# Kernel optimization log

Hardware: AMD Instinct MI355X
Metric: run time of the kernel (lower is better)

## Reference

```python
import jax, jax.numpy as jnp
import numpy as np

D_MODEL = 1024
BULK_DIM = 10          # int(log2(d_model))
ADS_RADIUS = 1.0
B, N = 4, 2048


def setup_inputs() -> dict:
    key = jax.random.key(0)
    k1, k2 = jax.random.split(key, 2)
    boundary_tokens = jax.random.normal(k1, (B, N, D_MODEL), dtype=jnp.float32)
    W_b2b = jax.random.normal(k2, (D_MODEL, D_MODEL * BULK_DIM), dtype=jnp.float32) / np.sqrt(D_MODEL).astype(np.float32)
    b_b2b = jnp.zeros((D_MODEL * BULK_DIM,), dtype=jnp.float32)
    return {"boundary_tokens": boundary_tokens, "W_b2b": W_b2b, "b_b2b": b_b2b}


def _fast_marching(bulk_coords, ads_radius):
    # bulk_coords: (B, N, K, D). Sequential eikonal-style sweep through the
    # bulk depth z = 1..K; AdS warp factor L/z attenuates the front update
    # deeper into the bulk. Returns geodesics with the same shape.
    cz = jnp.moveaxis(bulk_coords, 2, 0)                 # (K, B, N, D)
    z = jnp.arange(1, bulk_coords.shape[2] + 1, dtype=bulk_coords.dtype)
    factors = ads_radius / z                             # (K,)

    def step(g, inp):
        c, f = inp
        g_new = g + f * (c - g)
        return g_new, g_new

    _, geos = jax.lax.scan(step, cz[0], (cz, factors))   # (K, B, N, D)
    return jnp.moveaxis(geos, 0, 2)                      # (B, N, K, D)


def reference(boundary_tokens, W_b2b, b_b2b):
    Bb, Nn, D = boundary_tokens.shape
    # boundary -> bulk linear projection, reshaped to (B, N, bulk_dim, D)
    bulk_coords = (boundary_tokens @ W_b2b + b_b2b).reshape(Bb, Nn, BULK_DIM, D)
    geodesics = _fast_marching(bulk_coords, ADS_RADIUS)  # (B, N, K, D)
    bulk_features = geodesics.mean(axis=2)               # (B, N, D)
    return bulk_features
```

## Files before the change

kernel.cpp:

```cpp
#include <hip/hip_runtime.h>
#include <stdint.h>


static constexpr float FW[10] = {
    0.2928968253968254f, 0.1928968253968254f, 0.1428968253968254f,
    0.1095634920634921f, 0.0845634920634921f, 0.0645634920634921f,
    0.0478968253968254f, 0.0336111111111111f, 0.0211111111111111f,
    0.0100000000000000f};

typedef __attribute__((ext_vector_type(8))) short short8;
typedef __attribute__((ext_vector_type(4))) float floatx4;

__device__ inline unsigned int bf16pack2(float hi, float lo) {
    unsigned int uh = __float_as_uint(hi) + 0x8000u;
    unsigned int ul = __float_as_uint(lo) + 0x8000u;
    return __builtin_amdgcn_perm(uh, ul, 0x07060302u);
}

#define LDS_AS(p) ((__attribute__((address_space(3))) unsigned int*)(p))
#define GLB_AS(p) ((const __attribute__((address_space(1))) unsigned int*)(p))

__global__ __launch_bounds__(256) void fold_w(const float* __restrict__ W,
                                              unsigned short* __restrict__ Wt) {
    __shared__ float T[32 * 65];
    const int t = threadIdx.x;
    const int n0 = blockIdx.x * 64;
    const int k0 = blockIdx.y * 32;

#pragma unroll
    for (int s = 0; s < 2; ++s) {
        int slot = s * 256 + t;
        int r = slot >> 4;
        int c4 = (slot & 15) * 4;
        const float4* src = (const float4*)(W + (size_t)(k0 + r) * 10240 + n0 + c4);
        float4 acc = {0.f, 0.f, 0.f, 0.f};
#pragma unroll
        for (int j = 0; j < 10; ++j) {
            float4 v = src[j * 256];
            acc.x += FW[j] * v.x; acc.y += FW[j] * v.y;
            acc.z += FW[j] * v.z; acc.w += FW[j] * v.w;
        }
        T[r * 65 + c4 + 0] = acc.x;
        T[r * 65 + c4 + 1] = acc.y;
        T[r * 65 + c4 + 2] = acc.z;
        T[r * 65 + c4 + 3] = acc.w;
    }
    __syncthreads();
#pragma unroll
    for (int s = 0; s < 2; ++s) {
        int slot = s * 256 + t;
        int nl = slot >> 3;
        int k4 = (slot & 7) * 4;
        float f0 = T[(k4 + 0) * 65 + nl];
        float f1 = T[(k4 + 1) * 65 + nl];
        float f2 = T[(k4 + 2) * 65 + nl];
        float f3 = T[(k4 + 3) * 65 + nl];
        uint2 p;
        p.x = bf16pack2(f1, f0);
        p.y = bf16pack2(f3, f2);
        *(uint2*)(Wt + (size_t)(n0 + nl) * 1024 + k0 + k4) = p;
    }
}

__global__ __launch_bounds__(256) void fold_b(const float* __restrict__ b,
                                              float* __restrict__ beff) {
    const int t = threadIdx.x;
    const float4* src = (const float4*)b + t;
    float4 acc = {0.f, 0.f, 0.f, 0.f};
#pragma unroll
    for (int j = 0; j < 10; ++j) {
        float4 v = src[j * 256];
        acc.x += FW[j] * v.x; acc.y += FW[j] * v.y;
        acc.z += FW[j] * v.z; acc.w += FW[j] * v.w;
    }
    ((float4*)beff)[t] = acc;
}

__global__ __launch_bounds__(256) void cvt_bf16(const float* __restrict__ A,
                                                uint4* __restrict__ Ab) {
    size_t i = (size_t)blockIdx.x * 256 + threadIdx.x;
    const float4* src = (const float4*)A + i * 2;
    float4 a0 = src[0], a1 = src[1];
    uint4 p;
    p.x = bf16pack2(a0.y, a0.x);
    p.y = bf16pack2(a0.w, a0.z);
    p.z = bf16pack2(a1.y, a1.x);
    p.w = bf16pack2(a1.w, a1.z);
    Ab[i] = p;
}

__global__ __launch_bounds__(256) void gemm_bf16(const unsigned short* __restrict__ Ab,
                                                 const unsigned short* __restrict__ Wt,
                                                 const float* __restrict__ beff,
                                                 float* __restrict__ C) {
    __shared__ __align__(16) unsigned char As[16384];
    __shared__ __align__(16) unsigned char Bs[16384];

    const int t = threadIdx.x;
    const int lane = t & 63;
    const int w = t >> 6;
    const int quad = lane >> 4;
    const int l15 = lane & 15;
    const int wm = (w & 1) * 64;
    const int wn = (w >> 1) * 64;
    const int bm = blockIdx.x * 128;
    const int bn = blockIdx.y * 128;

    floatx4 acc[4][4];
#pragma unroll
    for (int i = 0; i < 4; ++i)
#pragma unroll
        for (int j = 0; j < 4; ++j) acc[i][j] = (floatx4){0.f, 0.f, 0.f, 0.f};

    const char* Abase = (const char*)Ab + (size_t)bm * 2048;
    const char* Bbase = (const char*)Wt + (size_t)bn * 2048;

    for (int k0 = 0; k0 < 1024; k0 += 64) {
#pragma unroll
        for (int i = 0; i < 4; ++i) {
            int I = w * 4 + i;
            int slot = I * 64 + lane;
            int m = slot >> 3;
            int c = (slot & 7) ^ (m & 7);
            size_t off = (size_t)m * 2048 + (size_t)k0 * 2 + c * 16;
            __builtin_amdgcn_global_load_lds(GLB_AS(Abase + off), LDS_AS(As + I * 1024), 16, 0, 0);
            __builtin_amdgcn_global_load_lds(GLB_AS(Bbase + off), LDS_AS(Bs + I * 1024), 16, 0, 0);
        }
        __syncthreads();

#pragma unroll
        for (int kk = 0; kk < 2; ++kk) {
            short8 af[4], bf[4];
            int c = kk * 4 + quad;
#pragma unroll
            for (int tm = 0; tm < 4; ++tm) {
                int m = wm + tm * 16 + l15;
                int slot = m * 8 + (c ^ (m & 7));
                af[tm] = *(const short8*)(As + slot * 16);
            }
#pragma unroll
            for (int tn = 0; tn < 4; ++tn) {
                int n = wn + tn * 16 + l15;
                int slot = n * 8 + (c ^ (n & 7));
                bf[tn] = *(const short8*)(Bs + slot * 16);
            }
#pragma unroll
            for (int tm = 0; tm < 4; ++tm)
#pragma unroll
                for (int tn = 0; tn < 4; ++tn)
                    acc[tm][tn] = __builtin_amdgcn_mfma_f32_16x16x32_bf16(
                        af[tm], bf[tn], acc[tm][tn], 0, 0, 0);
        }
        __syncthreads();
    }

#pragma unroll
    for (int tn = 0; tn < 4; ++tn) {
        int col = bn + wn + tn * 16 + l15;
        float bias = beff[col];
#pragma unroll
        for (int tm = 0; tm < 4; ++tm) {
            int row0 = bm + wm + tm * 16 + quad * 4;
#pragma unroll
            for (int r = 0; r < 4; ++r)
                C[(size_t)(row0 + r) * 1024 + col] = acc[tm][tn][r] + bias;
        }
    }
}

__global__ __launch_bounds__(256) void gemm_fb(const float* __restrict__ A,
                                               const unsigned short* __restrict__ Wt,
                                               const float* __restrict__ beff,
                                               float* __restrict__ C) {
    __shared__ __align__(16) unsigned short As[128 * 72];
    __shared__ __align__(16) unsigned char Bs[16384];

    const int t = threadIdx.x;
    const int lane = t & 63;
    const int w = t >> 6;
    const int quad = lane >> 4;
    const int l15 = lane & 15;
    const int wm = (w & 1) * 64;
    const int wn = (w >> 1) * 64;
    const int bm = blockIdx.y * 128;
    const int bn = blockIdx.x * 128;

    floatx4 acc[4][4];
#pragma unroll
    for (int i = 0; i < 4; ++i)
#pragma unroll
        for (int j = 0; j < 4; ++j) acc[i][j] = (floatx4){0.f, 0.f, 0.f, 0.f};

    const int ar = t >> 4;
    const int ac4 = (t & 15) * 4;
    const float* Abase = A + (size_t)(bm + ar) * 1024 + ac4;
    const char* WtB = (const char*)Wt;

    for (int k0 = 0; k0 < 1024; k0 += 64) {
#pragma unroll
        for (int i = 0; i < 4; ++i) {
            int I = w * 4 + i;
            int slot = I * 64 + lane;
            int nl = slot >> 3;
            int c = (slot & 7) ^ (nl & 7);
            const char* g = WtB + (size_t)(bn + nl) * 2048 + k0 * 2 + c * 16;
            __builtin_amdgcn_global_load_lds(GLB_AS(g), LDS_AS(Bs + I * 1024), 16, 0, 0);
        }
        float4 av[8];
#pragma unroll
        for (int s = 0; s < 8; ++s)
            av[s] = *(const float4*)(Abase + (size_t)(s * 16) * 1024 + k0);
#pragma unroll
        for (int s = 0; s < 8; ++s) {
            uint2 p;
            p.x = bf16pack2(av[s].y, av[s].x);
            p.y = bf16pack2(av[s].w, av[s].z);
            *(uint2*)((char*)As + (size_t)(s * 16 + ar) * 144 + ac4 * 2) = p;
        }
        __syncthreads();
#pragma unroll
        for (int kk = 0; kk < 2; ++kk) {
            short8 af[4], bf[4];
#pragma unroll
            for (int tm = 0; tm < 4; ++tm) {
                int m = wm + tm * 16 + l15;
                af[tm] = *(const short8*)((const char*)As + (size_t)m * 144 + kk * 64 + quad * 16);
            }
#pragma unroll
            for (int tn = 0; tn < 4; ++tn) {
                int n = wn + tn * 16 + l15;
                int c = kk * 4 + quad;
                int slot = n * 8 + (c ^ (n & 7));
                bf[tn] = *(const short8*)(Bs + slot * 16);
            }
#pragma unroll
            for (int tm = 0; tm < 4; ++tm)
#pragma unroll
                for (int tn = 0; tn < 4; ++tn)
                    acc[tm][tn] = __builtin_amdgcn_mfma_f32_16x16x32_bf16(
                        af[tm], bf[tn], acc[tm][tn], 0, 0, 0);
        }
        __syncthreads();
    }
#pragma unroll
    for (int tn = 0; tn < 4; ++tn) {
        int col = bn + wn + tn * 16 + l15;
        float bias = beff[col];
#pragma unroll
        for (int tm = 0; tm < 4; ++tm) {
            int row0 = bm + wm + tm * 16 + quad * 4;
#pragma unroll
            for (int r = 0; r < 4; ++r)
                C[(size_t)(row0 + r) * 1024 + col] = acc[tm][tn][r] + bias;
        }
    }
}

extern "C" void kernel_launch(void* const* d_in, const int* in_sizes, int n_in,
                              void* d_out, int out_size, void* d_ws, size_t ws_size,
                              hipStream_t stream) {
    const float* tokens = (const float*)d_in[0];
    const float* W      = (const float*)d_in[1];
    const float* b      = (const float*)d_in[2];
    float* out = (float*)d_out;

    unsigned short* Wt = (unsigned short*)d_ws;
    float* beff = (float*)((char*)d_ws + 2097152);
    unsigned short* Ab = (unsigned short*)((char*)d_ws + 2101248);

    fold_w<<<dim3(16, 32), 256, 0, stream>>>(W, Wt);
    fold_b<<<1, 256, 0, stream>>>(b, beff);

    if (ws_size >= 2101248 + (size_t)8192 * 1024 * 2) {
        cvt_bf16<<<4096, 256, 0, stream>>>(tokens, (uint4*)Ab);
        gemm_bf16<<<dim3(64, 8), 256, 0, stream>>>(Ab, Wt, beff, out);
    } else {
        gemm_fb<<<dim3(8, 64), 256, 0, stream>>>(tokens, Wt, beff, out);
    }
}
```

Before: 135.8 us.

## Merge prep kernels into one launch and switch GEMM to 32x32x16 MFMA

Folds the three preprocessing kernels (weight fold/transpose, bias fold, token bf16 conversion) into a single launch that dispatches on block index, removing two kernel launches. The GEMM moves from 16x16x32 to 32x32x16 bf16 MFMA tiles with 2x2 accumulators per wave, which halves the LDS fragment reads per MFMA and cuts the instruction count. In exchange, the epilogue stores are more scattered across rows, and the larger accumulators use more registers.

```diff
diff --git a/kernel.cpp b/kernel.cpp
--- a/kernel.cpp
+++ b/kernel.cpp
@@ -10,6 +10,7 @@
 
 typedef __attribute__((ext_vector_type(8))) short short8;
 typedef __attribute__((ext_vector_type(4))) float floatx4;
+typedef __attribute__((ext_vector_type(16))) float floatx16;
 
 __device__ inline unsigned int bf16pack2(float hi, float lo) {
     unsigned int uh = __float_as_uint(hi) + 0x8000u;
@@ -20,19 +21,57 @@
 #define LDS_AS(p) ((__attribute__((address_space(3))) unsigned int*)(p))
 #define GLB_AS(p) ((const __attribute__((address_space(1))) unsigned int*)(p))
 
-__global__ __launch_bounds__(256) void fold_w(const float* __restrict__ W,
-                                              unsigned short* __restrict__ Wt) {
+__global__ __launch_bounds__(256) void prep(const float* __restrict__ W,
+                                            const float* __restrict__ tokens,
+                                            const float* __restrict__ b,
+                                            unsigned short* __restrict__ Wt,
+                                            float* __restrict__ beff,
+                                            uint4* __restrict__ Ab,
+                                            int do_cvt) {
     __shared__ float T[32 * 65];
     const int t = threadIdx.x;
-    const int n0 = blockIdx.x * 64;
-    const int k0 = blockIdx.y * 32;
-
-#pragma unroll
-    for (int s = 0; s < 2; ++s) {
-        int slot = s * 256 + t;
-        int r = slot >> 4;
-        int c4 = (slot & 15) * 4;
-        const float4* src = (const float4*)(W + (size_t)(k0 + r) * 10240 + n0 + c4);
+    const int bid = blockIdx.x;
+
+    if (bid < 512) {
+        const int n0 = (bid & 15) * 64;
+        const int k0 = (bid >> 4) * 32;
+#pragma unroll
+        for (int s = 0; s < 2; ++s) {
+            int slot = s * 256 + t;
+            int r = slot >> 4;
+            int c4 = (slot & 15) * 4;
+            const float4* src = (const float4*)(W + (size_t)(k0 + r) * 10240 + n0 + c4);
+            float4 acc = {0.f, 0.f, 0.f, 0.f};
+#pragma unroll
+            for (int j = 0; j < 10; ++j) {
+                float4 v = src[j * 256];
+                acc.x += FW[j] * v.x; acc.y += FW[j] * v.y;
+                acc.z += FW[j] * v.z; acc.w += FW[j] * v.w;
+            }
+            T[r * 65 + c4 + 0] = acc.x;
+            T[r * 65 + c4 + 1] = acc.y;
+            T[r * 65 + c4 + 2] = acc.z;
+            T[r * 65 + c4 + 3] = acc.w;
+        }
+        __syncthreads();
+#pragma unroll
+        for (int s = 0; s < 2; ++s) {
+            int slot = s * 256 + t;
+            int nl = slot >> 3;
+            int k4 = (slot & 7) * 4;
+            float f0 = T[(k4 + 0) * 65 + nl];
+            float f1 = T[(k4 + 1) * 65 + nl];
+            float f2 = T[(k4 + 2) * 65 + nl];
+            float f3 = T[(k4 + 3) * 65 + nl];
+            uint2 p;
+            p.x = bf16pack2(f1, f0);
+            p.y = bf16pack2(f3, f2);
+            *(uint2*)(Wt + (size_t)(n0 + nl) * 1024 + k0 + k4) = p;
+        }
+        return;
+    }
+    if (bid == 512) {
+        const float4* src = (const float4*)b + t;
         float4 acc = {0.f, 0.f, 0.f, 0.f};
 #pragma unroll
         for (int j = 0; j < 10; ++j) {
@@ -40,77 +79,46 @@
             acc.x += FW[j] * v.x; acc.y += FW[j] * v.y;
             acc.z += FW[j] * v.z; acc.w += FW[j] * v.w;
         }
-        T[r * 65 + c4 + 0] = acc.x;
-        T[r * 65 + c4 + 1] = acc.y;
-        T[r * 65 + c4 + 2] = acc.z;
-        T[r * 65 + c4 + 3] = acc.w;
-    }
-    __syncthreads();
-#pragma unroll
-    for (int s = 0; s < 2; ++s) {
-        int slot = s * 256 + t;
-        int nl = slot >> 3;
-        int k4 = (slot & 7) * 4;
-        float f0 = T[(k4 + 0) * 65 + nl];
-        float f1 = T[(k4 + 1) * 65 + nl];
-        float f2 = T[(k4 + 2) * 65 + nl];
-        float f3 = T[(k4 + 3) * 65 + nl];
-        uint2 p;
-        p.x = bf16pack2(f1, f0);
-        p.y = bf16pack2(f3, f2);
-        *(uint2*)(Wt + (size_t)(n0 + nl) * 1024 + k0 + k4) = p;
-    }
-}
-
-__global__ __launch_bounds__(256) void fold_b(const float* __restrict__ b,
-                                              float* __restrict__ beff) {
-    const int t = threadIdx.x;
-    const float4* src = (const float4*)b + t;
-    float4 acc = {0.f, 0.f, 0.f, 0.f};
-#pragma unroll
-    for (int j = 0; j < 10; ++j) {
-        float4 v = src[j * 256];
-        acc.x += FW[j] * v.x; acc.y += FW[j] * v.y;
-        acc.z += FW[j] * v.z; acc.w += FW[j] * v.w;
-    }
-    ((float4*)beff)[t] = acc;
-}
-
-__global__ __launch_bounds__(256) void cvt_bf16(const float* __restrict__ A,
-                                                uint4* __restrict__ Ab) {
-    size_t i = (size_t)blockIdx.x * 256 + threadIdx.x;
-    const float4* src = (const float4*)A + i * 2;
-    float4 a0 = src[0], a1 = src[1];
-    uint4 p;
-    p.x = bf16pack2(a0.y, a0.x);
-    p.y = bf16pack2(a0.w, a0.z);
-    p.z = bf16pack2(a1.y, a1.x);
-    p.w = bf16pack2(a1.w, a1.z);
-    Ab[i] = p;
-}
-
-__global__ __launch_bounds__(256) void gemm_bf16(const unsigned short* __restrict__ Ab,
-                                                 const unsigned short* __restrict__ Wt,
-                                                 const float* __restrict__ beff,
-                                                 float* __restrict__ C) {
+        ((float4*)beff)[t] = acc;
+        return;
+    }
+    if (do_cvt) {
+        size_t i = (size_t)(bid - 513) * 256 + t;
+        const float4* src = (const float4*)tokens + i * 2;
+        float4 a0 = src[0], a1 = src[1];
+        uint4 p;
+        p.x = bf16pack2(a0.y, a0.x);
+        p.y = bf16pack2(a0.w, a0.z);
+        p.z = bf16pack2(a1.y, a1.x);
+        p.w = bf16pack2(a1.w, a1.z);
+        Ab[i] = p;
+    }
+}
+
+__global__ __launch_bounds__(256) void gemm32(const unsigned short* __restrict__ Ab,
+                                              const unsigned short* __restrict__ Wt,
+                                              const float* __restrict__ beff,
+                                              float* __restrict__ C) {
     __shared__ __align__(16) unsigned char As[16384];
     __shared__ __align__(16) unsigned char Bs[16384];
 
     const int t = threadIdx.x;
     const int lane = t & 63;
     const int w = t >> 6;
-    const int quad = lane >> 4;
-    const int l15 = lane & 15;
+    const int l31 = lane & 31;
+    const int khalf = lane >> 5;
     const int wm = (w & 1) * 64;
     const int wn = (w >> 1) * 64;
     const int bm = blockIdx.x * 128;
     const int bn = blockIdx.y * 128;
 
-    floatx4 acc[4][4];
-#pragma unroll
-    for (int i = 0; i < 4; ++i)
-#pragma unroll
-        for (int j = 0; j < 4; ++j) acc[i][j] = (floatx4){0.f, 0.f, 0.f, 0.f};
+    floatx16 acc[2][2];
+#pragma unroll
+    for (int i = 0; i < 2; ++i)
+#pragma unroll
+        for (int j = 0; j < 2; ++j)
+#pragma unroll
+            for (int r = 0; r < 16; ++r) acc[i][j][r] = 0.f;
 
     const char* Abase = (const char*)Ab + (size_t)bm * 2048;
     const char* Bbase = (const char*)Wt + (size_t)bn * 2048;
@@ -129,41 +137,43 @@
         __syncthreads();
 
 #pragma unroll
-        for (int kk = 0; kk < 2; ++kk) {
-            short8 af[4], bf[4];
-            int c = kk * 4 + quad;
-#pragma unroll
-            for (int tm = 0; tm < 4; ++tm) {
-                int m = wm + tm * 16 + l15;
+        for (int kk = 0; kk < 4; ++kk) {
+            int c = kk * 2 + khalf;
+            short8 af[2], bf[2];
+#pragma unroll
+            for (int tm = 0; tm < 2; ++tm) {
+                int m = wm + tm * 32 + l31;
                 int slot = m * 8 + (c ^ (m & 7));
                 af[tm] = *(const short8*)(As + slot * 16);
             }
 #pragma unroll
-            for (int tn = 0; tn < 4; ++tn) {
-                int n = wn + tn * 16 + l15;
+            for (int tn = 0; tn < 2; ++tn) {
+                int n = wn + tn * 32 + l31;
                 int slot = n * 8 + (c ^ (n & 7));
                 bf[tn] = *(const short8*)(Bs + slot * 16);
             }
 #pragma unroll
-            for (int tm = 0; tm < 4; ++tm)
-#pragma unroll
-                for (int tn = 0; tn < 4; ++tn)
-                    acc[tm][tn] = __builtin_amdgcn_mfma_f32_16x16x32_bf16(
+            for (int tm = 0; tm < 2; ++tm)
+#pragma unroll
+                for (int tn = 0; tn < 2; ++tn)
+                    acc[tm][tn] = __builtin_amdgcn_mfma_f32_32x32x16_bf16(
                         af[tm], bf[tn], acc[tm][tn], 0, 0, 0);
         }
         __syncthreads();
     }
 
 #pragma unroll
-    for (int tn = 0; tn < 4; ++tn) {
-        int col = bn + wn + tn * 16 + l15;
+    for (int tn = 0; tn < 2; ++tn) {
+        int col = bn + wn + tn * 32 + l31;
         float bias = beff[col];
 #pragma unroll
-        for (int tm = 0; tm < 4; ++tm) {
-            int row0 = bm + wm + tm * 16 + quad * 4;
-#pragma unroll
-            for (int r = 0; r < 4; ++r)
-                C[(size_t)(row0 + r) * 1024 + col] = acc[tm][tn][r] + bias;
+        for (int tm = 0; tm < 2; ++tm) {
+            int rbase = bm + wm + tm * 32 + 4 * khalf;
+#pragma unroll
+            for (int r = 0; r < 16; ++r) {
+                int row = rbase + (r & 3) + 8 * (r >> 2);
+                C[(size_t)row * 1024 + col] = acc[tm][tn][r] + bias;
+            }
         }
     }
 }
@@ -268,13 +278,13 @@
     float* beff = (float*)((char*)d_ws + 2097152);
     unsigned short* Ab = (unsigned short*)((char*)d_ws + 2101248);
 
-    fold_w<<<dim3(16, 32), 256, 0, stream>>>(W, Wt);
-    fold_b<<<1, 256, 0, stream>>>(b, beff);
-
-    if (ws_size >= 2101248 + (size_t)8192 * 1024 * 2) {
-        cvt_bf16<<<4096, 256, 0, stream>>>(tokens, (uint4*)Ab);
-        gemm_bf16<<<dim3(64, 8), 256, 0, stream>>>(Ab, Wt, beff, out);
+    const int big_ws = ws_size >= 2101248 + (size_t)8192 * 1024 * 2;
+
+    if (big_ws) {
+        prep<<<513 + 4096, 256, 0, stream>>>(W, tokens, b, Wt, beff, (uint4*)Ab, 1);
+        gemm32<<<dim3(64, 8), 256, 0, stream>>>(Ab, Wt, beff, out);
     } else {
+        prep<<<513, 256, 0, stream>>>(W, tokens, b, Wt, beff, (uint4*)Ab, 0);
         gemm_fb<<<dim3(8, 64), 256, 0, stream>>>(tokens, Wt, beff, out);
     }
 }
```

After: 131.0 us. -3.5%, faster.
